# Performance work log

Measured on AMD Instinct MI355X. Metric: run time of the kernel, lower is better.

The kernel has to match this reference:

```python
import jax, jax.numpy as jnp
import numpy as np
from functools import partial

VOCAB, D, H, L, T_MAX = 32000, 1024, 16, 8, 1024
HD = D // H
HIDDEN = int(D * 2.67)  # 2734, matches int(n_embd*hidden_mult)


def setup_inputs() -> dict:
    key = jax.random.key(0)
    ks = jax.random.split(key, 9)
    s = 0.02
    return {
        "idx": jax.random.randint(ks[0], (2, 1024), 0, VOCAB),
        "W_emb": jax.random.normal(ks[1], (VOCAB, D), jnp.float32) * s,  # tied with lm_head
        "norm1_w": jnp.ones((L, D), jnp.float32),
        "Wqkv": jax.random.normal(ks[2], (L, D, 3 * D), jnp.float32) * s,
        "Wout": jax.random.normal(ks[3], (L, D, D), jnp.float32) * s,
        "norm2_w": jnp.ones((L, D), jnp.float32),
        "Wg": jax.random.normal(ks[4], (L, D, HIDDEN), jnp.float32) * s,
        "Wu": jax.random.normal(ks[5], (L, D, HIDDEN), jnp.float32) * s,
        "Wd": jax.random.normal(ks[6], (L, HIDDEN, D), jnp.float32) * s,
        "final_norm_w": jnp.ones((D,), jnp.float32),
    }


def _rmsnorm(x, w, eps=1e-6):
    rms = jnp.sqrt(jnp.mean(x * x, axis=-1, keepdims=True) + eps)
    return x / rms * w


def _rope(x, cos_f, sin_f):
    # x: [B,H,T,hd]; cos_f/sin_f: [T, hd//2]
    x1, x2 = x[..., : HD // 2], x[..., HD // 2 :]
    c = cos_f[None, None]
    s = sin_f[None, None]
    return jnp.concatenate([x1 * c - x2 * s, x1 * s + x2 * c], axis=-1)


def _forward(idx, W_emb, norm1_w, Wqkv, Wout, norm2_w, Wg, Wu, Wd, final_norm_w):
    B, T = idx.shape
    # RoPE tables (buffers in the torch module)
    inv_freq = 1.0 / (10000.0 ** (jnp.arange(0, HD, 2, dtype=jnp.float32) / HD))
    ang = jnp.arange(T, dtype=jnp.float32)[:, None] * inv_freq[None, :]  # [T, hd//2]
    cos_f, sin_f = jnp.cos(ang), jnp.sin(ang)
    causal = jnp.tril(jnp.ones((T, T), dtype=bool))  # [T,T]
    scale = 1.0 / jnp.sqrt(jnp.float32(HD))

    def block(x, params):
        n1, wqkv, wout, n2, wg, wu, wd = params
        h = _rmsnorm(x, n1)
        qkv = (h @ wqkv).reshape(B, T, 3, H, HD).transpose(2, 0, 3, 1, 4)  # [3,B,H,T,hd]
        q, k, v = qkv[0], qkv[1], qkv[2]
        q = _rope(q, cos_f, sin_f)
        k = _rope(k, cos_f, sin_f)
        attn = jnp.einsum("bhqd,bhkd->bhqk", q, k) * scale
        attn = jnp.where(causal[None, None], attn, -jnp.inf)
        attn = jax.nn.softmax(attn, axis=-1)
        o = jnp.einsum("bhqk,bhkd->bhqd", attn, v)
        o = o.transpose(0, 2, 1, 3).reshape(B, T, D) @ wout
        x = x + o
        h2 = _rmsnorm(x, n2)
        x = x + (jax.nn.silu(h2 @ wg) * (h2 @ wu)) @ wd
        return x, None

    x = W_emb[idx]  # [B,T,D]
    x, _ = jax.lax.scan(block, x, (norm1_w, Wqkv, Wout, norm2_w, Wg, Wu, Wd))
    x = _rmsnorm(x, final_norm_w)
    return x @ W_emb.T  # tied lm_head -> [B,T,VOCAB]


def reference(idx, W_emb, norm1_w, Wqkv, Wout, norm2_w, Wg, Wu, Wd, final_norm_w):
    return _forward(idx, W_emb, norm1_w, Wqkv, Wout, norm2_w, Wg, Wu, Wd, final_norm_w)
```

## Files before the change

kernel.cpp:

```cpp
#include <hip/hip_runtime.h>
#include <cstdint>
#include <cmath>

#define D_MODEL 1024
#define T_SEQ   1024
#define NHEAD   16
#define NLAYER  8
#define HID     2734
#define HID_PAD 2816
#define NTOK    2048
#define VOCAB   32000

typedef __bf16 bf16x8 __attribute__((ext_vector_type(8)));
typedef __bf16 bf16x4 __attribute__((ext_vector_type(4)));
typedef float  f32x4  __attribute__((ext_vector_type(4)));

__device__ inline bf16x4 to_bf4(float a, float b, float c, float d) {
  bf16x4 t; t[0] = (__bf16)a; t[1] = (__bf16)b; t[2] = (__bf16)c; t[3] = (__bf16)d; return t;
}

__device__ inline void gload16(const __bf16* g, __bf16* l) {
  __builtin_amdgcn_global_load_lds(
      (const __attribute__((address_space(1))) void*)g,
      (__attribute__((address_space(3))) void*)l, 16, 0, 0);
}

__global__ __launch_bounds__(256) void embed_kernel(const int* __restrict__ idx,
                                                    const float* __restrict__ W,
                                                    float* __restrict__ x) {
  int t = blockIdx.x;
  int v = idx[t];
  float4 val = *(const float4*)&W[(size_t)v * D_MODEL + threadIdx.x * 4];
  *(float4*)&x[(size_t)t * D_MODEL + threadIdx.x * 4] = val;
}

__global__ __launch_bounds__(256) void rmsnorm_kernel(const float* __restrict__ x,
                                                      const float* __restrict__ w,
                                                      __bf16* __restrict__ out) {
  int row = blockIdx.x;
  int tid = threadIdx.x;
  float4 v = *(const float4*)&x[(size_t)row * D_MODEL + tid * 4];
  float s = v.x * v.x + v.y * v.y + v.z * v.z + v.w * v.w;
#pragma unroll
  for (int m = 32; m >= 1; m >>= 1) s += __shfl_xor(s, m, 64);
  __shared__ float red[4];
  if ((tid & 63) == 0) red[tid >> 6] = s;
  __syncthreads();
  float tot = red[0] + red[1] + red[2] + red[3];
  float inv = rsqrtf(tot * (1.0f / (float)D_MODEL) + 1e-6f);
  float4 wv = *(const float4*)&w[tid * 4];
  bf16x4 o4 = to_bf4(v.x * inv * wv.x, v.y * inv * wv.y, v.z * inv * wv.z, v.w * inv * wv.w);
  *(bf16x4*)&out[(size_t)row * D_MODEL + tid * 4] = o4;
}

__global__ __launch_bounds__(256) void rope_table_kernel(float* __restrict__ tab) {
  int p = blockIdx.x * 256 + threadIdx.x;
  int t = p >> 5, i = p & 31;
  float freq = exp2f(-(float)i * (13.287712379549449f / 32.0f));
  float sn, cs;
  sincosf((float)t * freq, &sn, &cs);
  tab[p] = cs;
  tab[32768 + p] = sn;
}

__global__ __launch_bounds__(256) void tp5_kernel(
    const float* __restrict__ Wqkv, const float* __restrict__ Wout,
    const float* __restrict__ Wg, const float* __restrict__ Wu,
    const float* __restrict__ Wd,
    __bf16* __restrict__ wqkvT, __bf16* __restrict__ woutT,
    __bf16* __restrict__ wguT, __bf16* __restrict__ wdT) {
  __shared__ __bf16 tile[64][65];
  int t = blockIdx.x;
  const float* in;
  __bf16* out;
  int R, C, Ro, rmul, roff, tr;
  if (t < 768)        { in = Wqkv; out = wqkvT; R = 1024; C = 3072; Ro = 1024; rmul = 1; roff = 0; tr = 16; }
  else if (t < 1024)  { t -= 768;  in = Wout; out = woutT; R = 1024; C = 1024; Ro = 1024; rmul = 1; roff = 0; tr = 16; }
  else if (t < 1728)  { t -= 1024; in = Wg; out = wguT; R = 1024; C = HID; Ro = 1024; rmul = 2; roff = 0; tr = 16; }
  else if (t < 2432)  { t -= 1728; in = Wu; out = wguT; R = 1024; C = HID; Ro = 1024; rmul = 2; roff = 1; tr = 16; }
  else                { t -= 2432; in = Wd; out = wdT; R = HID; C = 1024; Ro = HID_PAD; rmul = 1; roff = 0; tr = 44; }
  int r0 = (t % tr) * 64, c0 = (t / tr) * 64;
  int tid = threadIdx.x;
  bool fullc = (c0 + 64 <= C);
#pragma unroll
  for (int i = 0; i < 4; ++i) {
    int ri = i * 16 + (tid >> 4);
    int ci = (tid & 15) * 4;
    int r = r0 + ri;
    float4 v = {0.f, 0.f, 0.f, 0.f};
    if (r < R) {
      const float* p = in + (size_t)r * C + c0 + ci;
      if (fullc) {
        v = *(const float4*)p;
      } else {
        int c = c0 + ci;
        if (c + 0 < C) v.x = p[0];
        if (c + 1 < C) v.y = p[1];
        if (c + 2 < C) v.z = p[2];
        if (c + 3 < C) v.w = p[3];
      }
    }
    tile[ri][ci + 0] = (__bf16)v.x;
    tile[ri][ci + 1] = (__bf16)v.y;
    tile[ri][ci + 2] = (__bf16)v.z;
    tile[ri][ci + 3] = (__bf16)v.w;
  }
  __syncthreads();
#pragma unroll
  for (int i = 0; i < 4; ++i) {
    int oc = i * 16 + (tid >> 4);
    int orr = (tid & 15) * 4;
    bf16x4 tv;
    tv[0] = tile[orr + 0][oc];
    tv[1] = tile[orr + 1][oc];
    tv[2] = tile[orr + 2][oc];
    tv[3] = tile[orr + 3][oc];
    *(bf16x4*)&out[((size_t)(c0 + oc) * rmul + roff) * Ro + r0 + orr] = tv;
  }
}

__global__ __launch_bounds__(256) void convert_bf16_kernel(const float* __restrict__ in,
                                                           __bf16* __restrict__ out, int n4) {
  for (int i = blockIdx.x * 256 + threadIdx.x; i < n4; i += gridDim.x * 256) {
    float4 v = ((const float4*)in)[i];
    ((bf16x4*)out)[i] = to_bf4(v.x, v.y, v.z, v.w);
  }
}

template <int WM, int WN, int EPI>
__global__ __launch_bounds__(WM * WN * 64, 3) void gemmF(
    const __bf16* __restrict__ A, const __bf16* __restrict__ B,
    const float* __restrict__ Cin, void* __restrict__ Cout,
    int K, int ldc,
    const float* __restrict__ Tab, __bf16* __restrict__ Qr,
    __bf16* __restrict__ Kr, __bf16* __restrict__ Vt) {
  constexpr int BM = WM * 64, BN = WN * 64;
  constexpr int NTH = WM * WN * 64;
  constexpr int SLOT = (BM + BN) * 32;
  constexpr int LA = (BM * 32) / (NTH * 8);
  constexpr int LB = (BN * 32) / (NTH * 8);
  static_assert(LA + LB == 4, "vmcnt literal assumes 4 loads per stage event");
  __shared__ __align__(16) __bf16 lds[3 * SLOT];

  const int tid = threadIdx.x;
  const int lane = tid & 63, wid = tid >> 6;
  const int wr = wid / WN, wn = wid % WN;
  const int lr = lane & 15, lg = lane >> 4;

  const int gx = gridDim.x;
  const int nwg = gx * gridDim.y;
  const int orig = blockIdx.y * gx + blockIdx.x;
  const int q = nwg >> 3, r8 = nwg & 7;
  const int xcd = orig & 7, loc = orig >> 3;
  const int swz = ((xcd < r8) ? xcd * (q + 1) : r8 * (q + 1) + (xcd - r8) * q) + loc;
  const int brow = (swz % gx) * BM;
  const int bcol = (swz / gx) * BN;

  const __bf16* pAg[LA];
  const __bf16* pBg[LB];
  int opA[LA], opB[LB];
#pragma unroll
  for (int i = 0; i < LA; ++i) {
    int p = tid + i * NTH;
    int row = ((p >> 6) << 4) | (p & 15), j = (p >> 4) & 3;
    pAg[i] = A + (size_t)(brow + row) * K + j * 8;
    opA[i] = p * 8;
  }
#pragma unroll
  for (int i = 0; i < LB; ++i) {
    int p = tid + i * NTH;
    int row = ((p >> 6) << 4) | (p & 15), j = (p >> 4) & 3;
    pBg[i] = B + (size_t)(bcol + row) * K + j * 8;
    opB[i] = BM * 32 + p * 8;
  }

  const int nph = K >> 5;

  auto STAGE = [&](int ph) {
    int ps = ph < nph ? ph : nph - 1;
    int ko = ps * 32;
    __bf16* s = lds + (ph % 3) * SLOT;
#pragma unroll
    for (int i = 0; i < LA; ++i) gload16(pAg[i] + ko, s + opA[i]);
#pragma unroll
    for (int i = 0; i < LB; ++i) gload16(pBg[i] + ko, s + opB[i]);
  };

  f32x4 acc[4][4];
#pragma unroll
  for (int m = 0; m < 4; ++m)
#pragma unroll
    for (int n = 0; n < 4; ++n) acc[m][n] = (f32x4){0.f, 0.f, 0.f, 0.f};

  STAGE(0);
  STAGE(1);

  const int fragoff = lg * 128 + lr * 8;

  for (int ph = 0; ph < nph; ++ph) {
    asm volatile("s_waitcnt vmcnt(4)" ::: "memory");
    __builtin_amdgcn_sched_barrier(0);
    __builtin_amdgcn_s_barrier();
    __builtin_amdgcn_sched_barrier(0);
    STAGE(ph + 2);
    const __bf16* Sb = lds + (ph % 3) * SLOT;
    bf16x8 afr[4], bfr[4];
#pragma unroll
    for (int n = 0; n < 4; ++n)
      bfr[n] = *(const bf16x8*)(Sb + BM * 32 + (wn * 64 + n * 16) * 32 + fragoff);
#pragma unroll
    for (int m = 0; m < 4; ++m)
      afr[m] = *(const bf16x8*)(Sb + (wr * 64 + m * 16) * 32 + fragoff);
    asm volatile("s_waitcnt lgkmcnt(0)" ::: "memory");
    __builtin_amdgcn_sched_barrier(0);
    __builtin_amdgcn_s_setprio(1);
#pragma unroll
    for (int m = 0; m < 4; ++m)
#pragma unroll
      for (int n = 0; n < 4; ++n)
        acc[m][n] = __builtin_amdgcn_mfma_f32_16x16x32_bf16(afr[m], bfr[n], acc[m][n], 0, 0, 0);
    __builtin_amdgcn_s_setprio(0);
  }

  if constexpr (EPI == 5) {
    const int colw = bcol + wn * 64;
    const int secw = colw >> 10;
    const int h = (colw >> 6) & 15;
#pragma unroll
    for (int m = 0; m < 4; ++m) {
      int row0 = brow + wr * 64 + m * 16 + lg * 4;
      int bb = row0 >> 10;
      int t0 = row0 & 1023;
      int bh = bb * 16 + h;
      if (secw < 2) {
        __bf16* base = (secw == 0 ? Qr : Kr) + ((size_t)bh * T_SEQ + t0) * 64;
#pragma unroll
        for (int n = 0; n < 2; ++n) {
          int din = n * 16 + lr;
#pragma unroll
          for (int rr = 0; rr < 4; ++rr) {
            float a = acc[m][n][rr], b2 = acc[m][n + 2][rr];
            float cs = Tab[(t0 + rr) * 32 + din];
            float sn = Tab[32768 + (t0 + rr) * 32 + din];
            base[(size_t)rr * 64 + din]      = (__bf16)(a * cs - b2 * sn);
            base[(size_t)rr * 64 + din + 32] = (__bf16)(a * sn + b2 * cs);
          }
        }
      } else {
#pragma unroll
        for (int n = 0; n < 4; ++n) {
          int din = n * 16 + lr;
          bf16x4 pk;
#pragma unroll
          for (int rr = 0; rr < 4; ++rr) pk[rr] = (__bf16)acc[m][n][rr];
          *(bf16x4*)&Vt[((size_t)bh * 64 + din) * T_SEQ + t0] = pk;
        }
      }
    }
  } else {
#pragma unroll
    for (int m = 0; m < 4; ++m) {
#pragma unroll
      for (int n = 0; n < 4; ++n) {
#pragma unroll
        for (int rr = 0; rr < 4; ++rr) {
          int row = brow + wr * 64 + m * 16 + lg * 4 + rr;
          int col = bcol + wn * 64 + n * 16 + lr;
          size_t off = (size_t)row * ldc + col;
          float vv = acc[m][n][rr];
          if (EPI == 0) {
            ((float*)Cout)[off] = vv;
          } else {
            float uv = __shfl_xor(vv, 1);
            if ((lr & 1) == 0) {
              float r = vv / (1.f + __expf(-vv)) * uv;
              ((__bf16*)Cout)[(size_t)row * ldc + (col >> 1)] = (__bf16)r;
            }
          }
        }
      }
    }
  }
}

template <int BM, int BN, int WM, int WN>
__global__ __launch_bounds__(WM * WN * 64, 2) void gemm8(
    const __bf16* __restrict__ A, const __bf16* __restrict__ B,
    const float* __restrict__ Cin, float* __restrict__ Cout,
    int K, int ldc) {
  constexpr int NTH = WM * WN * 64;
  constexpr int MF = BM / (16 * WM);
  constexpr int MG = (MF + 3) / 4;
  constexpr int CL = (MF < 4) ? MF : 4;
  constexpr int LA = (BM * 4) / NTH;
  constexpr int LB = (BN * 4) / NTH;
  static_assert(BN / WN == 64, "NF must be 4");
  __shared__ __align__(16) __bf16 lds[(BM + BN) * 128];

  const int tid = threadIdx.x;
  const int lane = tid & 63, wid = tid >> 6;
  const int wr = wid / WN, wn = wid % WN;
  const int lr = lane & 15, lg = lane >> 4;

  const int gx = gridDim.x;
  const int nwg = gx * gridDim.y;
  const int orig = blockIdx.y * gx + blockIdx.x;
  const int q = nwg >> 3, r8 = nwg & 7;
  const int xcd = orig & 7, loc = orig >> 3;
  const int swz = ((xcd < r8) ? xcd * (q + 1) : r8 * (q + 1) + (xcd - r8) * q) + loc;
  const int brow = (swz % gx) * BM;
  const int bcol = (swz / gx) * BN;

  const __bf16* pAg[LA];
  const __bf16* pBg[LB];
  int opA[LA], opB[LB];
#pragma unroll
  for (int i = 0; i < LA; ++i) {
    int p = tid + i * NTH;
    int row = ((p >> 6) << 4) | (p & 15), j = (p >> 4) & 3;
    pAg[i] = A + (size_t)(brow + row) * K + j * 8;
    opA[i] = p * 8;
  }
#pragma unroll
  for (int i = 0; i < LB; ++i) {
    int p = tid + i * NTH;
    int row = ((p >> 6) << 4) | (p & 15), j = (p >> 4) & 3;
    pBg[i] = B + (size_t)(bcol + row) * K + j * 8;
    opB[i] = p * 8;
  }

  const int ntiles = K >> 6;

  auto STAGE_A = [&](int v, int kkq) {
    int vs = v < ntiles ? v : ntiles - 1;
    int ko = vs * 64 + kkq * 32;
    int sa = (v & 1) * (BM * 64) + kkq * (BM * 32);
#pragma unroll
    for (int i = 0; i < LA; ++i) gload16(pAg[i] + ko, lds + sa + opA[i]);
  };
  auto STAGE_B = [&](int v, int kkq) {
    int vs = v < ntiles ? v : ntiles - 1;
    int ko = vs * 64 + kkq * 32;
    int sb = BM * 128 + (v & 1) * (BN * 64) + kkq * (BN * 32);
#pragma unroll
    for (int i = 0; i < LB; ++i) gload16(pBg[i] + ko, lds + sb + opB[i]);
  };

  f32x4 acc[MF][4];
#pragma unroll
  for (int m = 0; m < MF; ++m)
#pragma unroll
    for (int n = 0; n < 4; ++n) acc[m][n] = (f32x4){0.f, 0.f, 0.f, 0.f};

  STAGE_A(0, 0); STAGE_B(0, 0);
  STAGE_A(0, 1); STAGE_B(0, 1);
  STAGE_A(1, 0); STAGE_B(1, 0);

  const int fragoff = lg * 128 + lr * 8;

  for (int u = 0; u < ntiles; ++u) {
    const int buf = u & 1;
#pragma unroll
    for (int kk = 0; kk < 2; ++kk) {
      if constexpr (LA + LB == 3) asm volatile("s_waitcnt vmcnt(6)" ::: "memory");
      else                        asm volatile("s_waitcnt vmcnt(8)" ::: "memory");
      __builtin_amdgcn_sched_barrier(0);
      __builtin_amdgcn_s_barrier();
      __builtin_amdgcn_sched_barrier(0);
      const int v = (kk == 0) ? u + 1 : u + 2;
      const int kkq = kk ^ 1;
      STAGE_A(v, kkq);
      STAGE_B(v, kkq);
      const __bf16* Ab = lds + buf * (BM * 64) + kk * (BM * 32);
      const __bf16* Bb = lds + BM * 128 + buf * (BN * 64) + kk * (BN * 32);
      bf16x8 bfr[4];
#pragma unroll
      for (int n = 0; n < 4; ++n)
        bfr[n] = *(const bf16x8*)(Bb + (wn * 64 + n * 16) * 32 + fragoff);
#pragma unroll
      for (int mg = 0; mg < MG; ++mg) {
        bf16x8 afr[CL];
#pragma unroll
        for (int i = 0; i < CL; ++i)
          afr[i] = *(const bf16x8*)(Ab + (wr * (BM / WM) + (mg * 4 + i) * 16) * 32 + fragoff);
        __builtin_amdgcn_s_setprio(1);
#pragma unroll
        for (int i = 0; i < CL; ++i)
#pragma unroll
          for (int n = 0; n < 4; ++n)
            acc[mg * 4 + i][n] =
                __builtin_amdgcn_mfma_f32_16x16x32_bf16(afr[i], bfr[n], acc[mg * 4 + i][n], 0, 0, 0);
        __builtin_amdgcn_s_setprio(0);
      }
    }
  }

#pragma unroll
  for (int m = 0; m < MF; ++m) {
#pragma unroll
    for (int n = 0; n < 4; ++n) {
#pragma unroll
      for (int rr = 0; rr < 4; ++rr) {
        int row = brow + wr * (BM / WM) + m * 16 + lg * 4 + rr;
        int col = bcol + wn * 64 + n * 16 + lr;
        size_t off = (size_t)row * ldc + col;
        Cout[off] = Cin[off] + acc[m][n][rr];
      }
    }
  }
}

__global__ __launch_bounds__(256) void attn_kernel(const __bf16* __restrict__ Qr,
                                                   const __bf16* __restrict__ Kr,
                                                   const __bf16* __restrict__ Vt,
                                                   __bf16* __restrict__ o) {
  __shared__ __align__(16) __bf16 lds[28672];
  const int tid = threadIdx.x;
  const int lane = tid & 63, w = tid >> 6;
  const int lr = lane & 15, lg = lane >> 4;
  const int bh = blockIdx.y, b = bh >> 4, h = bh & 15;
  const int qp = blockIdx.x;
  const __bf16* Kg = Kr + (size_t)bh * T_SEQ * 64;
  const __bf16* Vg = Vt + (size_t)bh * 64 * T_SEQ;
  const float scale = 0.125f;
  __bf16* Pw = lds + 20480 + w * 2048;

  for (int qs = 0; qs < 2; ++qs) {
    const int qb = qs ? (15 - qp) : qp;
    const int q0 = qb * 64;
    const __bf16* Qg = Qr + ((size_t)bh * T_SEQ + q0) * 64;

    __syncthreads();
    {
      int row = ((tid >> 6) << 4) | (tid & 15);
      int j = (tid >> 4) & 3;
      gload16(Qg + row * 64 + j * 8, lds + tid * 8);
      gload16(Qg + row * 64 + 32 + j * 8, lds + 2048 + tid * 8);
    }

    f32x4 accO[4];
#pragma unroll
    for (int n = 0; n < 4; ++n) accO[n] = (f32x4){0.f, 0.f, 0.f, 0.f};
    float mrow[4], lrow[4];
#pragma unroll
    for (int r = 0; r < 4; ++r) { mrow[r] = -1e30f; lrow[r] = 0.f; }

    const int ntile = ((q0 + 63) >> 7) + 1;

    for (int tt = 0; tt < ntile; ++tt) {
      const int j0 = tt * 128;
      __syncthreads();
#pragma unroll
      for (int i = 0; i < 2; ++i) {
        int p = tid + i * 256;
        int row = ((p >> 6) << 4) | (p & 15), j = (p >> 4) & 3;
        const __bf16* src = Kg + (size_t)(j0 + row) * 64 + j * 8;
        gload16(src, lds + 4096 + p * 8);
        gload16(src + 32, lds + 8192 + p * 8);
      }
#pragma unroll
      for (int s = 0; s < 4; ++s) {
        int d = ((tid >> 6) << 4) | (tid & 15), j = (tid >> 4) & 3;
        gload16(Vg + (size_t)d * T_SEQ + j0 + s * 32 + j * 8, lds + 12288 + s * 2048 + tid * 8);
      }
      __syncthreads();

      f32x4 s4[8];
#pragma unroll
      for (int n = 0; n < 8; ++n) s4[n] = (f32x4){0.f, 0.f, 0.f, 0.f};
#pragma unroll
      for (int kk = 0; kk < 2; ++kk) {
        bf16x8 aq = *(const bf16x8*)(lds + kk * 2048 + (w * 64 + lg * 16 + lr) * 8);
        __builtin_amdgcn_s_setprio(1);
#pragma unroll
        for (int jf = 0; jf < 8; ++jf) {
          bf16x8 bk = *(const bf16x8*)(lds + 4096 + kk * 4096 + (jf * 64 + lg * 16 + lr) * 8);
          s4[jf] = __builtin_amdgcn_mfma_f32_16x16x32_bf16(aq, bk, s4[jf], 0, 0, 0);
        }
        __builtin_amdgcn_s_setprio(0);
      }

      float pm[4];
#pragma unroll
      for (int r = 0; r < 4; ++r) pm[r] = -1e30f;
#pragma unroll
      for (int jf = 0; jf < 8; ++jf) {
        int gj = j0 + jf * 16 + lr;
#pragma unroll
        for (int r = 0; r < 4; ++r) {
          int gq = q0 + w * 16 + lg * 4 + r;
          float sv = s4[jf][r] * scale;
          if (gj > gq) sv = -1e30f;
          s4[jf][r] = sv;
          pm[r] = fmaxf(pm[r], sv);
        }
      }
#pragma unroll
      for (int r = 0; r < 4; ++r) {
#pragma unroll
        for (int m = 8; m >= 1; m >>= 1) pm[r] = fmaxf(pm[r], __shfl_xor(pm[r], m, 64));
      }
      float alpha[4];
#pragma unroll
      for (int r = 0; r < 4; ++r) {
        float mn = fmaxf(mrow[r], pm[r]);
        alpha[r] = expf(mrow[r] - mn);
        mrow[r] = mn;
      }
      float ps[4] = {0.f, 0.f, 0.f, 0.f};
#pragma unroll
      for (int jf = 0; jf < 8; ++jf) {
#pragma unroll
        for (int r = 0; r < 4; ++r) {
          float p = expf(s4[jf][r] - mrow[r]);
          s4[jf][r] = p;
          ps[r] += p;
        }
      }
#pragma unroll
      for (int r = 0; r < 4; ++r) {
#pragma unroll
        for (int m = 8; m >= 1; m >>= 1) ps[r] += __shfl_xor(ps[r], m, 64);
        lrow[r] = lrow[r] * alpha[r] + ps[r];
      }
#pragma unroll
      for (int n = 0; n < 4; ++n) {
#pragma unroll
        for (int r = 0; r < 4; ++r) accO[n][r] *= alpha[r];
      }

#pragma unroll
      for (int jf = 0; jf < 8; ++jf) {
        int s = jf >> 1;
        int rem = ((jf & 1) << 4) + lr;
        int base = s * 512 + (rem >> 3) * 128 + (rem & 7);
#pragma unroll
        for (int r = 0; r < 4; ++r) {
          int qloc = lg * 4 + r;
          Pw[base + qloc * 8] = (__bf16)s4[jf][r];
        }
      }
      asm volatile("s_waitcnt lgkmcnt(0)" ::: "memory");
      __builtin_amdgcn_sched_barrier(0);

#pragma unroll
      for (int s = 0; s < 4; ++s) {
        bf16x8 pa = *(const bf16x8*)(Pw + s * 512 + (lg * 16 + lr) * 8);
        __builtin_amdgcn_s_setprio(1);
#pragma unroll
        for (int nd = 0; nd < 4; ++nd) {
          bf16x8 bv = *(const bf16x8*)(lds + 12288 + s * 2048 + (nd * 64 + lg * 16 + lr) * 8);
          accO[nd] = __builtin_amdgcn_mfma_f32_16x16x32_bf16(pa, bv, accO[nd], 0, 0, 0);
        }
        __builtin_amdgcn_s_setprio(0);
      }
    }

#pragma unroll
    for (int nd = 0; nd < 4; ++nd) {
#pragma unroll
      for (int r = 0; r < 4; ++r) {
        int gq = q0 + w * 16 + lg * 4 + r;
        float val = accO[nd][r] / lrow[r];
        o[(size_t)(b * T_SEQ + gq) * D_MODEL + h * 64 + nd * 16 + lr] = (__bf16)val;
      }
    }
  }
}

extern "C" void kernel_launch(void* const* d_in, const int* in_sizes, int n_in,
                              void* d_out, int out_size, void* d_ws, size_t ws_size,
                              hipStream_t stream) {
  const int*   idx     = (const int*)d_in[0];
  const float* W_emb   = (const float*)d_in[1];
  const float* norm1_w = (const float*)d_in[2];
  const float* Wqkv    = (const float*)d_in[3];
  const float* Wout    = (const float*)d_in[4];
  const float* norm2_w = (const float*)d_in[5];
  const float* Wg      = (const float*)d_in[6];
  const float* Wu      = (const float*)d_in[7];
  const float* Wd      = (const float*)d_in[8];
  const float* fnorm   = (const float*)d_in[9];
  float* out = (float*)d_out;

  float*  x    = (float*)d_ws;
  float*  tab  = x + (size_t)NTOK * D_MODEL;
  __bf16* hb   = (__bf16*)(tab + 2 * 32768);
  __bf16* ob   = hb + (size_t)NTOK * D_MODEL;
  __bf16* ga   = ob + (size_t)NTOK * D_MODEL;
  __bf16* Qrb  = ga + (size_t)NTOK * HID_PAD;
  __bf16* Krb  = Qrb + (size_t)32 * T_SEQ * 64;
  __bf16* Vtb  = Krb + (size_t)32 * T_SEQ * 64;
  __bf16* wbuf = Vtb + (size_t)32 * T_SEQ * 64;

  __bf16* wqkvT = wbuf;
  __bf16* woutT = wqkvT + (size_t)3 * D_MODEL * D_MODEL;
  __bf16* wguT  = woutT + (size_t)D_MODEL * D_MODEL;
  __bf16* wdT   = wguT + (size_t)2 * HID_PAD * D_MODEL;

  embed_kernel<<<NTOK, 256, 0, stream>>>(idx, W_emb, x);
  rope_table_kernel<<<128, 256, 0, stream>>>(tab);

  for (int l = 0; l < NLAYER; ++l) {
    tp5_kernel<<<3136, 256, 0, stream>>>(
        Wqkv + (size_t)l * D_MODEL * 3 * D_MODEL,
        Wout + (size_t)l * D_MODEL * D_MODEL,
        Wg + (size_t)l * D_MODEL * HID,
        Wu + (size_t)l * D_MODEL * HID,
        Wd + (size_t)l * HID * D_MODEL,
        wqkvT, woutT, wguT, wdT);

    rmsnorm_kernel<<<NTOK, 256, 0, stream>>>(x, norm1_w + (size_t)l * D_MODEL, hb);
    gemmF<2, 2, 5><<<dim3(16, 24), 256, 0, stream>>>(
        hb, wqkvT, nullptr, nullptr, D_MODEL, 3 * D_MODEL, tab, Qrb, Krb, Vtb);
    attn_kernel<<<dim3(8, 32), 256, 0, stream>>>(Qrb, Krb, Vtb, ob);
    gemm8<128, 64, 4, 1><<<dim3(16, 16), 256, 0, stream>>>(
        ob, woutT, x, x, D_MODEL, D_MODEL);
    rmsnorm_kernel<<<NTOK, 256, 0, stream>>>(x, norm2_w + (size_t)l * D_MODEL, hb);
    gemmF<2, 2, 4><<<dim3(16, 44), 256, 0, stream>>>(
        hb, wguT, nullptr, ga, D_MODEL, HID_PAD, nullptr, nullptr, nullptr, nullptr);
    gemm8<128, 64, 4, 1><<<dim3(16, 16), 256, 0, stream>>>(
        ga, wdT, x, x, HID_PAD, D_MODEL);
  }

  rmsnorm_kernel<<<NTOK, 256, 0, stream>>>(x, fnorm, hb);
  convert_bf16_kernel<<<2048, 256, 0, stream>>>(W_emb, wbuf, VOCAB * D_MODEL / 4);
  gemmF<2, 2, 0><<<dim3(16, 250), 256, 0, stream>>>(
      hb, wbuf, nullptr, out, D_MODEL, VOCAB, nullptr, nullptr, nullptr, nullptr);
}
```

Baseline: 1.943 ms.

## Replace gemmF with 8-wave larger-tile GEMM using 4-stage LDS and fragment double-buffering

Replaces the 4-wave 128x128 GEMM with an 8-wave kernel using 128x256 or 256x128 tiles, a 4-slot LDS ring and register double-buffered fragments. LDS reads for the next k-step are issued while the current step's MFMAs run. This aims to hide LDS and global latency and raise operand reuse per tile. It costs a larger LDS footprint, higher register pressure and fewer workgroups (192 for QKV, 352 for gate/up), which may underfill the GPU.

```diff
diff --git a/kernel.cpp b/kernel.cpp
--- a/kernel.cpp
+++ b/kernel.cpp
@@ -127,20 +127,22 @@
   }
 }
 
-template <int WM, int WN, int EPI>
-__global__ __launch_bounds__(WM * WN * 64, 3) void gemmF(
+template <int BM, int BN, int WM, int WN, int EPI>
+__global__ __launch_bounds__(512, 2) void gemmM(
     const __bf16* __restrict__ A, const __bf16* __restrict__ B,
-    const float* __restrict__ Cin, void* __restrict__ Cout,
-    int K, int ldc,
+    void* __restrict__ Cout, int K, int ldc,
     const float* __restrict__ Tab, __bf16* __restrict__ Qr,
     __bf16* __restrict__ Kr, __bf16* __restrict__ Vt) {
-  constexpr int BM = WM * 64, BN = WN * 64;
   constexpr int NTH = WM * WN * 64;
+  static_assert(NTH == 512, "8 waves");
+  constexpr int MF = BM / (16 * WM);
+  static_assert(MF == 4, "frag double-buffer sized for MF=4");
+  static_assert(BN / WN == 64, "NF must be 4");
   constexpr int SLOT = (BM + BN) * 32;
-  constexpr int LA = (BM * 32) / (NTH * 8);
-  constexpr int LB = (BN * 32) / (NTH * 8);
-  static_assert(LA + LB == 4, "vmcnt literal assumes 4 loads per stage event");
-  __shared__ __align__(16) __bf16 lds[3 * SLOT];
+  constexpr int LA = BM / 128;
+  constexpr int LB = BN / 128;
+  static_assert(LA + LB == 3, "vmcnt literals assume 3 loads/stage event");
+  __shared__ __align__(16) __bf16 lds[4 * SLOT];
 
   const int tid = threadIdx.x;
   const int lane = tid & 63, wid = tid >> 6;
@@ -174,52 +176,71 @@
     opB[i] = BM * 32 + p * 8;
   }
 
-  const int nph = K >> 5;
-
-  auto STAGE = [&](int ph) {
-    int ps = ph < nph ? ph : nph - 1;
-    int ko = ps * 32;
-    __bf16* s = lds + (ph % 3) * SLOT;
+  const int P = K >> 5;
+  const int fragoff = lg * 128 + lr * 8;
+
+  auto STAGE = [&](int p) {
+    int pc = p < P ? p : P - 1;
+    int ko = pc * 32;
+    __bf16* s = lds + (p & 3) * SLOT;
 #pragma unroll
     for (int i = 0; i < LA; ++i) gload16(pAg[i] + ko, s + opA[i]);
 #pragma unroll
     for (int i = 0; i < LB; ++i) gload16(pBg[i] + ko, s + opB[i]);
   };
-
-  f32x4 acc[4][4];
-#pragma unroll
-  for (int m = 0; m < 4; ++m)
+  auto READS = [&](int p, bf16x8 (&af)[MF], bf16x8 (&bf)[4]) {
+    int pc = p < P ? p : P - 1;
+    const __bf16* Sb = lds + (pc & 3) * SLOT;
+#pragma unroll
+    for (int n = 0; n < 4; ++n)
+      bf[n] = *(const bf16x8*)(Sb + BM * 32 + (wn * 64 + n * 16) * 32 + fragoff);
+#pragma unroll
+    for (int m = 0; m < MF; ++m)
+      af[m] = *(const bf16x8*)(Sb + (wr * (BM / WM) + m * 16) * 32 + fragoff);
+  };
+
+  f32x4 acc[MF][4];
+#pragma unroll
+  for (int m = 0; m < MF; ++m)
 #pragma unroll
     for (int n = 0; n < 4; ++n) acc[m][n] = (f32x4){0.f, 0.f, 0.f, 0.f};
 
-  STAGE(0);
-  STAGE(1);
-
-  const int fragoff = lg * 128 + lr * 8;
-
-  for (int ph = 0; ph < nph; ++ph) {
-    asm volatile("s_waitcnt vmcnt(4)" ::: "memory");
+  auto DOMFMA = [&](bf16x8 (&af)[MF], bf16x8 (&bf)[4]) {
+    __builtin_amdgcn_s_setprio(1);
+#pragma unroll
+    for (int m = 0; m < MF; ++m)
+#pragma unroll
+      for (int n = 0; n < 4; ++n)
+        acc[m][n] = __builtin_amdgcn_mfma_f32_16x16x32_bf16(af[m], bf[n], acc[m][n], 0, 0, 0);
+    __builtin_amdgcn_s_setprio(0);
+  };
+
+  bf16x8 fA[MF], bA[4], fB[MF], bB[4];
+
+  STAGE(0); STAGE(1); STAGE(2);
+  asm volatile("s_waitcnt vmcnt(6)" ::: "memory");
+  __builtin_amdgcn_sched_barrier(0);
+  __builtin_amdgcn_s_barrier();
+  __builtin_amdgcn_sched_barrier(0);
+  READS(0, fA, bA);
+
+  for (int p = 0; p < P; p += 2) {
+    asm volatile("s_waitcnt vmcnt(3)" ::: "memory");
     __builtin_amdgcn_sched_barrier(0);
     __builtin_amdgcn_s_barrier();
-    __builtin_amdgcn_sched_barrier(0);
-    STAGE(ph + 2);
-    const __bf16* Sb = lds + (ph % 3) * SLOT;
-    bf16x8 afr[4], bfr[4];
-#pragma unroll
-    for (int n = 0; n < 4; ++n)
-      bfr[n] = *(const bf16x8*)(Sb + BM * 32 + (wn * 64 + n * 16) * 32 + fragoff);
-#pragma unroll
-    for (int m = 0; m < 4; ++m)
-      afr[m] = *(const bf16x8*)(Sb + (wr * 64 + m * 16) * 32 + fragoff);
     asm volatile("s_waitcnt lgkmcnt(0)" ::: "memory");
     __builtin_amdgcn_sched_barrier(0);
-    __builtin_amdgcn_s_setprio(1);
-#pragma unroll
-    for (int m = 0; m < 4; ++m)
-#pragma unroll
-      for (int n = 0; n < 4; ++n)
-        acc[m][n] = __builtin_amdgcn_mfma_f32_16x16x32_bf16(afr[m], bfr[n], acc[m][n], 0, 0, 0);
-    __builtin_amdgcn_s_setprio(0);
+    STAGE(p + 3);
+    DOMFMA(fA, bA);
+    READS(p + 1, fB, bB);
+    asm volatile("s_waitcnt vmcnt(3)" ::: "memory");
+    __builtin_amdgcn_sched_barrier(0);
+    __builtin_amdgcn_s_barrier();
+    asm volatile("s_waitcnt lgkmcnt(0)" ::: "memory");
+    __builtin_amdgcn_sched_barrier(0);
+    STAGE(p + 4);
+    DOMFMA(fB, bB);
+    READS(p + 2, fA, bA);
   }
 
   if constexpr (EPI == 5) {
@@ -227,8 +248,8 @@
     const int secw = colw >> 10;
     const int h = (colw >> 6) & 15;
 #pragma unroll
-    for (int m = 0; m < 4; ++m) {
-      int row0 = brow + wr * 64 + m * 16 + lg * 4;
+    for (int m = 0; m < MF; ++m) {
+      int row0 = brow + wr * (BM / WM) + m * 16 + lg * 4;
       int bb = row0 >> 10;
       int t0 = row0 & 1023;
       int bh = bb * 16 + h;
@@ -259,12 +280,12 @@
     }
   } else {
 #pragma unroll
-    for (int m = 0; m < 4; ++m) {
+    for (int m = 0; m < MF; ++m) {
 #pragma unroll
       for (int n = 0; n < 4; ++n) {
 #pragma unroll
         for (int rr = 0; rr < 4; ++rr) {
-          int row = brow + wr * 64 + m * 16 + lg * 4 + rr;
+          int row = brow + wr * (BM / WM) + m * 16 + lg * 4 + rr;
           int col = bcol + wn * 64 + n * 16 + lr;
           size_t off = (size_t)row * ldc + col;
           float vv = acc[m][n][rr];
@@ -611,20 +632,20 @@
         wqkvT, woutT, wguT, wdT);
 
     rmsnorm_kernel<<<NTOK, 256, 0, stream>>>(x, norm1_w + (size_t)l * D_MODEL, hb);
-    gemmF<2, 2, 5><<<dim3(16, 24), 256, 0, stream>>>(
-        hb, wqkvT, nullptr, nullptr, D_MODEL, 3 * D_MODEL, tab, Qrb, Krb, Vtb);
+    gemmM<128, 256, 2, 4, 5><<<dim3(16, 12), 512, 0, stream>>>(
+        hb, wqkvT, nullptr, D_MODEL, 3 * D_MODEL, tab, Qrb, Krb, Vtb);
     attn_kernel<<<dim3(8, 32), 256, 0, stream>>>(Qrb, Krb, Vtb, ob);
     gemm8<128, 64, 4, 1><<<dim3(16, 16), 256, 0, stream>>>(
         ob, woutT, x, x, D_MODEL, D_MODEL);
     rmsnorm_kernel<<<NTOK, 256, 0, stream>>>(x, norm2_w + (size_t)l * D_MODEL, hb);
-    gemmF<2, 2, 4><<<dim3(16, 44), 256, 0, stream>>>(
-        hb, wguT, nullptr, ga, D_MODEL, HID_PAD, nullptr, nullptr, nullptr, nullptr);
+    gemmM<128, 256, 2, 4, 4><<<dim3(16, 22), 512, 0, stream>>>(
+        hb, wguT, ga, D_MODEL, HID_PAD, nullptr, nullptr, nullptr, nullptr);
     gemm8<128, 64, 4, 1><<<dim3(16, 16), 256, 0, stream>>>(
         ga, wdT, x, x, HID_PAD, D_MODEL);
   }
 
   rmsnorm_kernel<<<NTOK, 256, 0, stream>>>(x, fnorm, hb);
   convert_bf16_kernel<<<2048, 256, 0, stream>>>(W_emb, wbuf, VOCAB * D_MODEL / 4);
-  gemmF<2, 2, 0><<<dim3(16, 250), 256, 0, stream>>>(
-      hb, wbuf, nullptr, out, D_MODEL, VOCAB, nullptr, nullptr, nullptr, nullptr);
-}
+  gemmM<256, 128, 4, 2, 0><<<dim3(8, 250), 512, 0, stream>>>(
+      hb, wbuf, out, D_MODEL, VOCAB, nullptr, nullptr, nullptr, nullptr);
+}
```

Result: no change. 1.906 ms (-1.9%).
